# Performance work log

Measured on AMD Instinct MI355X. Metric: run time of the kernel, lower is better.

Reference implementation:

```python
import jax, jax.numpy as jnp
import numpy as np

EPS = 1e-5


def _conv1x1(w, x):
    # w: [O, C, 1, 1], x: [B, C, H, W] -> [B, O, H, W]
    return jnp.einsum('oc,bchw->bohw', w[:, :, 0, 0], x)


def _bn_train(y, g, b):
    # BatchNorm2d in training mode: batch statistics over (B, H, W)
    m = y.mean(axis=(0, 2, 3), keepdims=True)
    v = y.var(axis=(0, 2, 3), keepdims=True)
    return (y - m) * jax.lax.rsqrt(v + EPS) * g[None, :, None, None] + b[None, :, None, None]


def setup_inputs() -> dict:
    key = jax.random.key(0)
    ks = jax.random.split(key, 8)
    B, C, H, W = 16, 512, 32, 32
    width, heads, hd, out_ch = 128, 4, 32, 512  # out_chans*expansion = 512
    return {
        'x': jax.random.normal(ks[0], (B, C, H, W), jnp.float32),
        'conv1_w': jax.random.normal(ks[1], (width, C, 1, 1), jnp.float32) * 0.05,
        'bn1_g': jnp.ones((width,), jnp.float32),
        'bn1_b': jnp.zeros((width,), jnp.float32),
        'qkv_w': jax.random.normal(ks[2], (3 * width, width, 1, 1), jnp.float32) * 0.05,
        'rw': jax.random.normal(ks[3], (1, heads, hd, 1, W), jnp.float32),
        'rh': jax.random.normal(ks[4], (1, heads, hd, H, 1), jnp.float32),
        'conv2_w': jax.random.normal(ks[5], (out_ch, width, 1, 1), jnp.float32) * 0.05,
        'bn2_g': jnp.ones((out_ch,), jnp.float32),
        'bn2_b': jnp.zeros((out_ch,), jnp.float32),
    }


def reference(x, conv1_w, bn1_g, bn1_b, qkv_w, rw, rh, conv2_w, bn2_g, bn2_b):
    B, C, H, W = x.shape
    heads = rw.shape[1]
    width = qkv_w.shape[1]
    hd = width // heads
    scale = hd ** (-0.5)
    N = H * W

    identity = x
    # conv1 = BaseConv: 1x1 conv (no bias) + BN + ReLU
    y = jax.nn.relu(_bn_train(_conv1x1(conv1_w, x), bn1_g, bn1_b))

    # Attention with relative position bias
    qkv = _conv1x1(qkv_w, y)                       # [B, 3*width, H, W]
    qkv = qkv.reshape(B, 3, heads, hd, N)          # split channels as (3, heads, hd)
    q, k, v = qkv[:, 0], qkv[:, 1], qkv[:, 2]      # each [B, heads, hd, N]

    attn_content = jnp.einsum('bhdn,bhdm->bhnm', q, k) * scale  # [B, heads, N, N]
    r = (rw + rh).reshape(heads, hd, N)                          # [heads, hd, N]
    attn_position = jnp.einsum('bhdn,hdm->bhnm', q, r) * scale
    attn = jax.nn.softmax(attn_content + attn_position, axis=-1)
    out = jnp.einsum('bhnm,bhdm->bhdn', attn, v)   # [B, heads, hd, N]
    y = out.reshape(B, width, H, W)

    # conv2 + BN, residual add, ReLU (stride==1: no pooling, no down_sample)
    y = _bn_train(_conv1x1(conv2_w, y), bn2_g, bn2_b)
    y = y + identity
    return jax.nn.relu(y)
```

## Files before the change

### kernel.cpp

```cpp
#include <hip/hip_runtime.h>
#include <cstddef>
#include <cstdint>

constexpr int BATCH = 16;
constexpr int NQ    = 1024;
constexpr float QSCALE = 0.17677669529663687f * 1.4426950408889634f;

typedef __attribute__((ext_vector_type(8))) short bf8;
typedef __attribute__((ext_vector_type(4))) float f32x4;
typedef __attribute__((ext_vector_type(4))) unsigned short us4;
typedef __attribute__((ext_vector_type(8))) unsigned short us8;

__device__ inline unsigned short f2bf(float x) {
  union { float f; uint32_t u; } c{x};
  uint32_t r = c.u + 0x7fffu + ((c.u >> 16) & 1u);
  return (unsigned short)(r >> 16);
}
__device__ inline float b2f(unsigned short v) {
  union { uint32_t u; float f; } c{(uint32_t)v << 16};
  return c.f;
}
__device__ inline float fast_exp2(float x) {
#if __has_builtin(__builtin_amdgcn_exp2f)
  return __builtin_amdgcn_exp2f(x);
#else
  return exp2f(x);
#endif
}

__global__ __launch_bounds__(256) void k_wcvt(const float* __restrict__ w1,
                                              const float* __restrict__ wq,
                                              const float* __restrict__ w2,
                                              unsigned short* __restrict__ o1,
                                              unsigned short* __restrict__ oq,
                                              unsigned short* __restrict__ o2) {
  int idx = (blockIdx.x * 256 + threadIdx.x) * 8;
  const float* s; unsigned short* d; int off;
  if (idx < 65536)        { s = w1; d = o1; off = idx; }
  else if (idx < 114688)  { s = wq; d = oq; off = idx - 65536; }
  else                    { s = w2; d = o2; off = idx - 114688; }
  float4 a = *(const float4*)(s + off);
  float4 b = *(const float4*)(s + off + 4);
  us8 o = {f2bf(a.x), f2bf(a.y), f2bf(a.z), f2bf(a.w),
           f2bf(b.x), f2bf(b.y), f2bf(b.z), f2bf(b.w)};
  *(us8*)(d + off) = o;
}

__global__ __launch_bounds__(256) void k_conv1(const float* __restrict__ x,
                                               const unsigned short* __restrict__ W,
                                               unsigned short* __restrict__ y1T) {
  constexpr int BS = 68;
  __shared__ unsigned short Bl[64 * BS];

  const int bb = blockIdx.z;
  const int n0 = blockIdx.x * 64;
  const int tid = threadIdx.x, lane = tid & 63, wv = tid >> 6;
  const int wn = wv & 1, wm = wv >> 1;
  const int i = lane & 15, g = lane >> 4;

  const int kb = tid >> 4, nb = tid & 15;

  f32x4 acc[2][4];
#pragma unroll
  for (int a = 0; a < 2; ++a)
#pragma unroll
    for (int b = 0; b < 4; ++b) acc[a][b] = {0.f, 0.f, 0.f, 0.f};

  float4 rv[4];
#pragma unroll
  for (int r = 0; r < 4; ++r)
    rv[r] = *(const float4*)(x + (((size_t)(bb * 512 + kb * 4 + r)) << 10) + n0 + nb * 4);

  for (int s = 0; s < 8; ++s) {
    bf8 wf[4][2];
#pragma unroll
    for (int b = 0; b < 4; ++b)
#pragma unroll
      for (int h = 0; h < 2; ++h)
        wf[b][h] = *(const bf8*)(W + (size_t)(wm * 64 + b * 16 + i) * 512 + s * 64 + h * 32 + g * 8);

    __syncthreads();
#pragma unroll
    for (int j = 0; j < 4; ++j) {
      us4 pk = {f2bf((&rv[0].x)[j]), f2bf((&rv[1].x)[j]),
                f2bf((&rv[2].x)[j]), f2bf((&rv[3].x)[j])};
      *(us4*)&Bl[(nb * 4 + j) * BS + kb * 4] = pk;
    }
    __syncthreads();

    if (s < 7) {
#pragma unroll
      for (int r = 0; r < 4; ++r)
        rv[r] = *(const float4*)(x + (((size_t)(bb * 512 + (s + 1) * 64 + kb * 4 + r)) << 10) + n0 + nb * 4);
    }

#pragma unroll
    for (int h = 0; h < 2; ++h) {
      bf8 af[2];
#pragma unroll
      for (int a = 0; a < 2; ++a)
        af[a] = *(const bf8*)&Bl[(wn * 32 + a * 16 + i) * BS + h * 32 + g * 8];
#pragma unroll
      for (int a = 0; a < 2; ++a)
#pragma unroll
        for (int b = 0; b < 4; ++b)
          acc[a][b] = __builtin_amdgcn_mfma_f32_16x16x32_bf16(wf[b][h], af[a], acc[a][b], 0, 0, 0);
    }
  }

#pragma unroll
  for (int a = 0; a < 2; ++a)
#pragma unroll
    for (int b = 0; b < 4; ++b) {
      const int n = n0 + wn * 32 + a * 16 + i;
      const int c = wm * 64 + b * 16 + 4 * g;
      us4 pk = {f2bf(acc[a][b][0]), f2bf(acc[a][b][1]), f2bf(acc[a][b][2]), f2bf(acc[a][b][3])};
      *(us4*)(y1T + ((size_t)(bb << 10) + n) * 128 + c) = pk;
    }
}

template<int KTOT, int MODE>
__global__ __launch_bounds__(256) void k_mm(const unsigned short* __restrict__ W,
                                            const unsigned short* __restrict__ Bact,
                                            const float* __restrict__ scl,
                                            const float* __restrict__ sht,
                                            const float* __restrict__ rw,
                                            const float* __restrict__ rh,
                                            unsigned short* __restrict__ out0,
                                            unsigned short* __restrict__ out1,
                                            unsigned short* __restrict__ out2) {
  constexpr int BS = 136;
  __shared__ unsigned short Blds[128 * BS];
  __shared__ float scl_s[128], sht_s[128];

  const int bb = blockIdx.z, mt = blockIdx.y;
  const int n0 = blockIdx.x * 128, m0 = mt * 64;
  const int tid = threadIdx.x, lane = tid & 63, wv = tid >> 6;
  const int wn = wv & 1, wm = wv >> 1;
  const int i = lane & 15, g = lane >> 4;

  const unsigned short* Bp = Bact + ((size_t)bb * NQ + n0) * KTOT;

  f32x4 acc[4][2];
#pragma unroll
  for (int a = 0; a < 4; ++a)
#pragma unroll
    for (int b = 0; b < 2; ++b) acc[a][b] = {0.f, 0.f, 0.f, 0.f};

  const int sn = tid >> 1;
  const int sk = (tid & 1) * 8;

  if (tid < 128) { scl_s[tid] = scl[tid]; sht_s[tid] = sht[tid]; }
  bf8 wf[2][4];
#pragma unroll
  for (int b = 0; b < 2; ++b)
#pragma unroll
    for (int h = 0; h < 4; ++h)
      wf[b][h] = *(const bf8*)(W + (size_t)(m0 + wm * 32 + b * 16 + i) * 128 + h * 32 + g * 8);
  __syncthreads();
#pragma unroll
  for (int p = 0; p < 8; ++p) {
    us8 v = *(const us8*)(Bp + (size_t)sn * 128 + sk + p * 16);
    const int kb = sk + p * 16;
    float scv[8], shv[8];
    *(float4*)scv = *(const float4*)&scl_s[kb];
    *(float4*)(scv + 4) = *(const float4*)&scl_s[kb + 4];
    *(float4*)shv = *(const float4*)&sht_s[kb];
    *(float4*)(shv + 4) = *(const float4*)&sht_s[kb + 4];
#pragma unroll
    for (int j = 0; j < 8; ++j)
      v[j] = f2bf(fmaxf(fmaf(b2f(v[j]), scv[j], shv[j]), 0.f));
    *(us8*)(&Blds[sn * BS + sk + p * 16]) = v;
  }
  __syncthreads();

  const bool actA = (mt >= 4);
  if (actA) {
#pragma unroll
    for (int h = 0; h < 4; ++h) {
      bf8 af[4];
#pragma unroll
      for (int a = 0; a < 4; ++a)
        af[a] = *(const bf8*)&Blds[(wn * 64 + a * 16 + i) * BS + h * 32 + g * 8];
#pragma unroll
      for (int a = 0; a < 4; ++a)
#pragma unroll
        for (int b = 0; b < 2; ++b)
          acc[a][b] = __builtin_amdgcn_mfma_f32_16x16x32_bf16(af[a], wf[b][h], acc[a][b], 0, 0, 0);
    }
  } else {
#pragma unroll
    for (int h = 0; h < 4; ++h) {
      bf8 af[4];
#pragma unroll
      for (int a = 0; a < 4; ++a)
        af[a] = *(const bf8*)&Blds[(wn * 64 + a * 16 + i) * BS + h * 32 + g * 8];
#pragma unroll
      for (int a = 0; a < 4; ++a)
#pragma unroll
        for (int b = 0; b < 2; ++b)
          acc[a][b] = __builtin_amdgcn_mfma_f32_16x16x32_bf16(wf[b][h], af[a], acc[a][b], 0, 0, 0);
    }
  }

  if (mt < 2) {
#pragma unroll
    for (int a = 0; a < 4; ++a)
#pragma unroll
      for (int b = 0; b < 2; ++b) {
        const int n = n0 + wn * 64 + a * 16 + i;
        const int c = m0 + wm * 32 + b * 16 + 4 * g;
        const int hh = c >> 5, d = c & 31;
        us4 pk = {f2bf(acc[a][b][0] * QSCALE), f2bf(acc[a][b][1] * QSCALE),
                  f2bf(acc[a][b][2] * QSCALE), f2bf(acc[a][b][3] * QSCALE)};
        *(us4*)(out0 + (((size_t)(bb * 4 + hh) << 10) + n) * 32 + d) = pk;
      }
  } else if (mt < 4) {
#pragma unroll
    for (int a = 0; a < 4; ++a)
#pragma unroll
      for (int b = 0; b < 2; ++b) {
        const int n = n0 + wn * 64 + a * 16 + i;
        const int c = (m0 - 128) + wm * 32 + b * 16 + 4 * g;
        const int hh = c >> 5, d = c & 31;
        const int wcol = n & 31, hrow = n >> 5;
        float vv[4];
#pragma unroll
        for (int r = 0; r < 4; ++r)
          vv[r] = acc[a][b][r] + rw[(c + r) * 32 + wcol] + rh[(c + r) * 32 + hrow];
        us4 pk = {f2bf(vv[0]), f2bf(vv[1]), f2bf(vv[2]), f2bf(vv[3])};
        *(us4*)(out1 + (((size_t)(bb * 4 + hh) << 10) + n) * 32 + d) = pk;
      }
  } else {
#pragma unroll
    for (int a = 0; a < 4; ++a)
#pragma unroll
      for (int b = 0; b < 2; ++b) {
        const int c = (m0 - 256) + wm * 32 + b * 16 + i;
        const int nb = n0 + wn * 64 + a * 16 + 4 * g;
        const int hh = c >> 5, dd = c & 31;
        us4 pk = {f2bf(acc[a][b][0]), f2bf(acc[a][b][1]), f2bf(acc[a][b][2]), f2bf(acc[a][b][3])};
        *(us4*)(out2 + (((size_t)(bb * 4 + hh) * 32 + dd) << 10) + nb) = pk;
      }
  }
}

__global__ __launch_bounds__(256) void k_mm2(const unsigned short* __restrict__ W,
                                             const float* __restrict__ Aof,
                                             float* __restrict__ y2,
                                             float* __restrict__ pBS,
                                             float* __restrict__ pBQ) {
  constexpr int BS = 264;
  __shared__ unsigned short Blds[64 * BS];
  __shared__ float Sl[256], Ql[256];
  const int bb = blockIdx.z;
  const int mh = blockIdx.y;
  const int n0 = blockIdx.x * 64;
  const int tid = threadIdx.x, lane = tid & 63, wv = tid >> 6;
  const int wn = wv & 1, wm = wv >> 1;
  const int i = lane & 15, g = lane >> 4;

  Sl[tid] = 0.f; Ql[tid] = 0.f;

  const int sn = tid >> 2, sk = (tid & 3) * 32;
  const float* src = Aof + (((size_t)(bb << 10)) + n0 + sn) * 128 + sk;
#pragma unroll
  for (int p = 0; p < 4; ++p) {
    float4 f0 = *(const float4*)(src + p * 8);
    float4 f1 = *(const float4*)(src + p * 8 + 4);
    float fv[8] = {f0.x, f0.y, f0.z, f0.w, f1.x, f1.y, f1.z, f1.w};
    us8 hi, lo;
#pragma unroll
    for (int j = 0; j < 8; ++j) {
      unsigned short h16 = f2bf(fv[j]);
      hi[j] = h16;
      lo[j] = f2bf(fv[j] - b2f(h16));
    }
    *(us8*)&Blds[sn * BS + sk + p * 8]       = hi;
    *(us8*)&Blds[sn * BS + 128 + sk + p * 8] = lo;
  }
  __syncthreads();

  auto loadw = [&](bf8 (&wf)[2][4], int lp) {
    const int mt = mh * 4 + lp;
#pragma unroll
    for (int b = 0; b < 2; ++b)
#pragma unroll
      for (int h = 0; h < 4; ++h)
        wf[b][h] = *(const bf8*)(W + (size_t)(mt * 64 + wm * 32 + b * 16 + i) * 128 + h * 32 + g * 8);
  };

  auto step = [&](bf8 (&wf)[2][4], int lp) {
    const int mt = mh * 4 + lp;
    f32x4 acc[2][2];
#pragma unroll
    for (int a = 0; a < 2; ++a)
#pragma unroll
      for (int b = 0; b < 2; ++b) acc[a][b] = {0.f, 0.f, 0.f, 0.f};
#pragma unroll
    for (int h = 0; h < 4; ++h) {
      bf8 ah[2], al[2];
#pragma unroll
      for (int a = 0; a < 2; ++a) {
        ah[a] = *(const bf8*)&Blds[(wn * 32 + a * 16 + i) * BS + h * 32 + g * 8];
        al[a] = *(const bf8*)&Blds[(wn * 32 + a * 16 + i) * BS + 128 + h * 32 + g * 8];
      }
#pragma unroll
      for (int a = 0; a < 2; ++a)
#pragma unroll
        for (int b = 0; b < 2; ++b) {
          acc[a][b] = __builtin_amdgcn_mfma_f32_16x16x32_bf16(ah[a], wf[b][h], acc[a][b], 0, 0, 0);
          acc[a][b] = __builtin_amdgcn_mfma_f32_16x16x32_bf16(al[a], wf[b][h], acc[a][b], 0, 0, 0);
        }
    }
#pragma unroll
    for (int a = 0; a < 2; ++a)
#pragma unroll
      for (int b = 0; b < 2; ++b) {
        const int c = mt * 64 + wm * 32 + b * 16 + i;
        const int nb = n0 + wn * 32 + a * 16 + 4 * g;
        *(f32x4*)(y2 + (((size_t)(bb * 512 + c)) << 10) + nb) = acc[a][b];
      }
#pragma unroll
    for (int b = 0; b < 2; ++b) {
      float s = 0.f, q = 0.f;
#pragma unroll
      for (int a = 0; a < 2; ++a)
#pragma unroll
        for (int r = 0; r < 4; ++r) {
          float v = acc[a][b][r];
          s += v; q += v * v;
        }
      s += __shfl_xor(s, 16); s += __shfl_xor(s, 32);
      q += __shfl_xor(q, 16); q += __shfl_xor(q, 32);
      if ((lane & 48) == 0) {
        const int cl = lp * 64 + wm * 32 + b * 16 + i;
        atomicAdd(&Sl[cl], s);
        atomicAdd(&Ql[cl], q);
      }
    }
  };

  bf8 wfA[2][4], wfB[2][4];
  loadw(wfA, 0);
#pragma unroll
  for (int mp = 0; mp < 2; ++mp) {
    loadw(wfB, 2 * mp + 1);
    step(wfA, 2 * mp);
    if (mp < 1) loadw(wfA, 2 * mp + 2);
    step(wfB, 2 * mp + 1);
  }

  __syncthreads();
  const int pidx = bb * 16 + blockIdx.x;
  pBS[(size_t)(mh * 256 + tid) * 256 + pidx] = Sl[tid];
  pBQ[(size_t)(mh * 256 + tid) * 256 + pidx] = Ql[tid];
}

__global__ __launch_bounds__(256) void k_bnstat1a(const unsigned short* __restrict__ y1T,
                                                  float* __restrict__ pS,
                                                  float* __restrict__ pQ) {
  const int blk = blockIdx.x, t = threadIdx.x;
  const int rr = t >> 4, co = t & 15;
  float s[8], q[8];
#pragma unroll
  for (int j = 0; j < 8; ++j) { s[j] = 0.f; q[j] = 0.f; }
  for (int it = 0; it < 16; ++it) {
    const int r = blk * 256 + rr + it * 16;
    us8 v = *(const us8*)(y1T + (size_t)r * 128 + co * 8);
#pragma unroll
    for (int j = 0; j < 8; ++j) { float f = b2f(v[j]); s[j] += f; q[j] += f * f; }
  }
  __shared__ float rs[16][16][8], rq[16][16][8];
#pragma unroll
  for (int j = 0; j < 8; ++j) { rs[rr][co][j] = s[j]; rq[rr][co][j] = q[j]; }
  __syncthreads();
  if (t < 128) {
    const int c = t;
    float S = 0.f, Q = 0.f;
    for (int r2 = 0; r2 < 16; ++r2) { S += rs[r2][c >> 3][c & 7]; Q += rq[r2][c >> 3][c & 7]; }
    pS[c * 64 + blk] = S;
    pQ[c * 64 + blk] = Q;
  }
}

__global__ __launch_bounds__(128) void k_bnfin1(const float* __restrict__ pS,
                                                const float* __restrict__ pQ,
                                                const float* __restrict__ g,
                                                const float* __restrict__ be,
                                                float* __restrict__ scl,
                                                float* __restrict__ sht) {
  const int c = threadIdx.x;
  float S = 0.f, Q = 0.f;
  for (int k = 0; k < 64; ++k) { S += pS[c * 64 + k]; Q += pQ[c * 64 + k]; }
  const float inv_n = 1.f / 16384.f;
  const float mean = S * inv_n, var = Q * inv_n - mean * mean;
  const float sc = rsqrtf(var + 1e-5f) * g[c];
  scl[c] = sc;
  sht[c] = be[c] - mean * sc;
}

__global__ __launch_bounds__(64) void k_bnfin2(const float* __restrict__ pBS,
                                               const float* __restrict__ pBQ,
                                               const float* __restrict__ g,
                                               const float* __restrict__ be,
                                               float* __restrict__ scl,
                                               float* __restrict__ sht) {
  const int c = blockIdx.x, t = threadIdx.x;
  float S = 0.f, Q = 0.f;
#pragma unroll
  for (int k = 0; k < 4; ++k) {
    S += pBS[(size_t)c * 256 + t + k * 64];
    Q += pBQ[(size_t)c * 256 + t + k * 64];
  }
#pragma unroll
  for (int o = 32; o > 0; o >>= 1) {
    S += __shfl_down(S, o);
    Q += __shfl_down(Q, o);
  }
  if (t == 0) {
    const float inv_n = 1.f / 16384.f;
    const float mean = S * inv_n, var = Q * inv_n - mean * mean;
    const float sc = rsqrtf(var + 1e-5f) * g[c];
    scl[c] = sc;
    sht[c] = be[c] - mean * sc;
  }
}

__global__ __launch_bounds__(256) void k_attn_mfma(const unsigned short* __restrict__ qs,
                                                   const unsigned short* __restrict__ kt,
                                                   const unsigned short* __restrict__ vt,
                                                   float* __restrict__ aoT) {
  const int bh   = blockIdx.y;
  const int tid  = threadIdx.x;
  const int lane = tid & 63;
  const int wv   = tid >> 6;
  const int i    = lane & 15;
  const int g    = lane >> 4;
  const int n0w  = blockIdx.x * 64 + wv * 16;

  __shared__ unsigned short Ks[64 * 56];
  __shared__ unsigned short Vt[32 * 72];

  const bf8 qf = *reinterpret_cast<const bf8*>(
      qs + ((size_t)bh * NQ + n0w + i) * 32 + g * 8);

  f32x4 o0 = {0.f, 0.f, 0.f, 0.f}, o1 = {0.f, 0.f, 0.f, 0.f};
  float m = -1e30f, lsum = 0.f;

  const unsigned short* kb = kt + (size_t)bh * NQ * 32;
  const unsigned short* vb = vt + (size_t)bh * 32 * NQ;

  const int skey = tid >> 2, sds = (tid & 3) * 8;
  const int svd  = tid >> 3, svn = (tid & 7) * 8;

  for (int k0 = 0; k0 < NQ; k0 += 64) {
    bf8 kvld = *reinterpret_cast<const bf8*>(kb + (size_t)(k0 + skey) * 32 + sds);
    bf8 vvld = *reinterpret_cast<const bf8*>(vb + (size_t)svd * NQ + k0 + svn);
    __syncthreads();
    *reinterpret_cast<bf8*>(&Ks[skey * 56 + sds]) = kvld;
    *reinterpret_cast<bf8*>(&Vt[svd * 72 + svn])  = vvld;
    __syncthreads();

    f32x4 st[4];
    const f32x4 zero = {0.f, 0.f, 0.f, 0.f};
#pragma unroll
    for (int t = 0; t < 4; ++t) {
      bf8 kf = *reinterpret_cast<const bf8*>(&Ks[(t * 16 + i) * 56 + g * 8]);
      st[t] = __builtin_amdgcn_mfma_f32_16x16x32_bf16(kf, qf, zero, 0, 0, 0);
    }

    float tmax = st[0][0];
#pragma unroll
    for (int t = 0; t < 4; ++t)
#pragma unroll
      for (int r = 0; r < 4; ++r) tmax = fmaxf(tmax, st[t][r]);
    tmax = fmaxf(tmax, __shfl_xor(tmax, 16));
    tmax = fmaxf(tmax, __shfl_xor(tmax, 32));

    const float mn   = fmaxf(m, tmax);
    const float corr = fast_exp2(m - mn);
    m = mn;

    float ps = 0.f;
    unsigned int pk[4][2];
#pragma unroll
    for (int t = 0; t < 4; ++t) {
      float p0 = fast_exp2(st[t][0] - mn);
      float p1 = fast_exp2(st[t][1] - mn);
      float p2 = fast_exp2(st[t][2] - mn);
      float p3 = fast_exp2(st[t][3] - mn);
      ps += (p0 + p1) + (p2 + p3);
      unsigned int pa, pb;
      asm("v_cvt_pk_bf16_f32 %0, %1, %2" : "=v"(pa) : "v"(p0), "v"(p1));
      asm("v_cvt_pk_bf16_f32 %0, %1, %2" : "=v"(pb) : "v"(p2), "v"(p3));
      pk[t][0] = pa; pk[t][1] = pb;
    }
    ps += __shfl_xor(ps, 16);
    ps += __shfl_xor(ps, 32);
    lsum = lsum * corr + ps;
#pragma unroll
    for (int r = 0; r < 4; ++r) { o0[r] *= corr; o1[r] *= corr; }

    const int src0 = ((g & 1) << 5) + i;
    const int src1 = src0 + 16;
    const bool hi = (g >= 2);
#pragma unroll
    for (int s = 0; s < 2; ++s) {
      int a0 = __shfl((int)pk[2 * s][0], src0);
      int a1 = __shfl((int)pk[2 * s][1], src0);
      int a2 = __shfl((int)pk[2 * s][0], src1);
      int a3 = __shfl((int)pk[2 * s][1], src1);
      int b0 = __shfl((int)pk[2 * s + 1][0], src0);
      int b1 = __shfl((int)pk[2 * s + 1][1], src0);
      int b2 = __shfl((int)pk[2 * s + 1][0], src1);
      int b3 = __shfl((int)pk[2 * s + 1][1], src1);
      union { int d[4]; bf8 v; } pf;
      pf.d[0] = hi ? b0 : a0;
      pf.d[1] = hi ? b1 : a1;
      pf.d[2] = hi ? b2 : a2;
      pf.d[3] = hi ? b3 : a3;
      bf8 vf0 = *reinterpret_cast<const bf8*>(&Vt[(i)      * 72 + s * 32 + g * 8]);
      bf8 vf1 = *reinterpret_cast<const bf8*>(&Vt[(16 + i) * 72 + s * 32 + g * 8]);
      o0 = __builtin_amdgcn_mfma_f32_16x16x32_bf16(vf0, pf.v, o0, 0, 0, 0);
      o1 = __builtin_amdgcn_mfma_f32_16x16x32_bf16(vf1, pf.v, o1, 0, 0, 0);
    }
  }

  const float inv = 1.f / lsum;
  float* dst = aoT + (((size_t)(bh >> 2) << 10) + n0w + i) * 128 + (bh & 3) * 32 + 4 * g;
  f32x4 p0 = {o0[0] * inv, o0[1] * inv, o0[2] * inv, o0[3] * inv};
  f32x4 p1 = {o1[0] * inv, o1[1] * inv, o1[2] * inv, o1[3] * inv};
  *(f32x4*)dst        = p0;
  *(f32x4*)(dst + 16) = p1;
}

__global__ __launch_bounds__(256) void k_final(const float* __restrict__ y2,
                                               const float* __restrict__ x,
                                               const float* __restrict__ scl,
                                               const float* __restrict__ sht,
                                               float* __restrict__ out) {
  const size_t idx = ((size_t)blockIdx.x * 256 + threadIdx.x) * 8;
  const int c = (int)((idx >> 10) & 511);
  const float sc = scl[c], sh = sht[c];
  float4 v0 = *(const float4*)(y2 + idx);
  float4 v1 = *(const float4*)(y2 + idx + 4);
  float4 x0 = *(const float4*)(x + idx);
  float4 x1 = *(const float4*)(x + idx + 4);
  float4 o0, o1;
  o0.x = fmaxf(v0.x * sc + sh + x0.x, 0.f);
  o0.y = fmaxf(v0.y * sc + sh + x0.y, 0.f);
  o0.z = fmaxf(v0.z * sc + sh + x0.z, 0.f);
  o0.w = fmaxf(v0.w * sc + sh + x0.w, 0.f);
  o1.x = fmaxf(v1.x * sc + sh + x1.x, 0.f);
  o1.y = fmaxf(v1.y * sc + sh + x1.y, 0.f);
  o1.z = fmaxf(v1.z * sc + sh + x1.z, 0.f);
  o1.w = fmaxf(v1.w * sc + sh + x1.w, 0.f);
  *(float4*)(out + idx)     = o0;
  *(float4*)(out + idx + 4) = o1;
}

extern "C" void kernel_launch(void* const* d_in, const int* in_sizes, int n_in,
                              void* d_out, int out_size, void* d_ws, size_t ws_size,
                              hipStream_t stream) {
  (void)in_sizes; (void)n_in; (void)out_size; (void)ws_size;
  const float* x    = (const float*)d_in[0];
  const float* w1   = (const float*)d_in[1];
  const float* g1   = (const float*)d_in[2];
  const float* b1   = (const float*)d_in[3];
  const float* wqkv = (const float*)d_in[4];
  const float* rw   = (const float*)d_in[5];
  const float* rh   = (const float*)d_in[6];
  const float* w2   = (const float*)d_in[7];
  const float* g2   = (const float*)d_in[8];
  const float* b2   = (const float*)d_in[9];
  float* out = (float*)d_out;
  char* base = (char*)d_ws;

  float*          y2  = (float*)(base);
  unsigned short* y1T = (unsigned short*)(base + (32u << 20));
  unsigned short* qs  = (unsigned short*)(base + (36u << 20));
  unsigned short* kt  = (unsigned short*)(base + (40u << 20));
  unsigned short* vt  = (unsigned short*)(base + (44u << 20));
  float*          aoT = (float*)(base + (48u << 20));
  unsigned short* wb1 = (unsigned short*)(base + (56u << 20));
  unsigned short* wbq = wb1 + 65536;
  unsigned short* wb2 = wbq + 49152;
  float* pS   = (float*)(base + (57u << 20));
  float* pQ   = pS + 8192;
  float* pBS  = pQ + 8192;
  float* pBQ  = pBS + 131072;
  float* scl1 = pBQ + 131072;
  float* sht1 = scl1 + 128;
  float* scl2 = sht1 + 128;
  float* sht2 = scl2 + 512;

  k_wcvt<<<88, 256, 0, stream>>>(w1, wqkv, w2, wb1, wbq, wb2);
  k_conv1<<<dim3(16, 1, BATCH), 256, 0, stream>>>(x, wb1, y1T);
  k_bnstat1a<<<64, 256, 0, stream>>>(y1T, pS, pQ);
  k_bnfin1<<<1, 128, 0, stream>>>(pS, pQ, g1, b1, scl1, sht1);
  k_mm<128, 1><<<dim3(8, 6, BATCH), 256, 0, stream>>>(wbq, y1T, scl1, sht1,
                                                      rw, rh, qs, kt, vt);
  k_attn_mfma<<<dim3(NQ / 64, BATCH * 4), 256, 0, stream>>>(qs, kt, vt, aoT);
  k_mm2<<<dim3(16, 2, BATCH), 256, 0, stream>>>(wb2, aoT, y2, pBS, pBQ);
  k_bnfin2<<<512, 64, 0, stream>>>(pBS, pBQ, g2, b2, scl2, sht2);
  k_final<<<4096, 256, 0, stream>>>(y2, x, scl2, sht2, out);
}
```

Measured before the change: 111.5 us.

## Fuse BN1 stats into conv1 and recompute conv2 to drop y2 buffer

BN1 partial sums are now computed in the conv1 epilogue from the bf16-rounded outputs, which removes the separate k_bnstat1a pass over y1T and parallelises bnfin1 across channels. The conv2 GEMM is run twice: once only for BN2 statistics, and again in a final kernel that applies BN2, the residual and ReLU directly. This avoids writing and re-reading the 32 MB fp32 y2 intermediate. The cost is doubling the conv2 split-bf16 MFMA work and the aoT reads.

```diff
diff --git a/kernel.cpp b/kernel.cpp
--- a/kernel.cpp
+++ b/kernel.cpp
@@ -48,9 +48,12 @@
 
 __global__ __launch_bounds__(256) void k_conv1(const float* __restrict__ x,
                                                const unsigned short* __restrict__ W,
-                                               unsigned short* __restrict__ y1T) {
+                                               unsigned short* __restrict__ y1T,
+                                               float* __restrict__ pS1,
+                                               float* __restrict__ pQ1) {
   constexpr int BS = 68;
   __shared__ unsigned short Bl[64 * BS];
+  __shared__ float Sl[128], Ql[128];
 
   const int bb = blockIdx.z;
   const int n0 = blockIdx.x * 64;
@@ -58,6 +61,8 @@
   const int wn = wv & 1, wm = wv >> 1;
   const int i = lane & 15, g = lane >> 4;
 
+  if (tid < 128) { Sl[tid] = 0.f; Ql[tid] = 0.f; }
+
   const int kb = tid >> 4, nb = tid & 15;
 
   f32x4 acc[2][4];
@@ -117,18 +122,79 @@
       us4 pk = {f2bf(acc[a][b][0]), f2bf(acc[a][b][1]), f2bf(acc[a][b][2]), f2bf(acc[a][b][3])};
       *(us4*)(y1T + ((size_t)(bb << 10) + n) * 128 + c) = pk;
     }
-}
-
-template<int KTOT, int MODE>
-__global__ __launch_bounds__(256) void k_mm(const unsigned short* __restrict__ W,
-                                            const unsigned short* __restrict__ Bact,
-                                            const float* __restrict__ scl,
-                                            const float* __restrict__ sht,
-                                            const float* __restrict__ rw,
-                                            const float* __restrict__ rh,
-                                            unsigned short* __restrict__ out0,
-                                            unsigned short* __restrict__ out1,
-                                            unsigned short* __restrict__ out2) {
+
+#pragma unroll
+  for (int b = 0; b < 4; ++b) {
+    float sb[4], qb[4];
+#pragma unroll
+    for (int r = 0; r < 4; ++r) {
+      float v0 = b2f(f2bf(acc[0][b][r]));
+      float v1 = b2f(f2bf(acc[1][b][r]));
+      sb[r] = v0 + v1;
+      qb[r] = v0 * v0 + v1 * v1;
+    }
+#pragma unroll
+    for (int o = 1; o < 16; o <<= 1) {
+#pragma unroll
+      for (int r = 0; r < 4; ++r) {
+        sb[r] += __shfl_xor(sb[r], o);
+        qb[r] += __shfl_xor(qb[r], o);
+      }
+    }
+    if (i == 0) {
+#pragma unroll
+      for (int r = 0; r < 4; ++r) {
+        const int c = wm * 64 + b * 16 + 4 * g + r;
+        atomicAdd(&Sl[c], sb[r]);
+        atomicAdd(&Ql[c], qb[r]);
+      }
+    }
+  }
+
+  __syncthreads();
+  const int blk = bb * 16 + blockIdx.x;
+  if (tid < 128) {
+    pS1[(size_t)tid * 256 + blk] = Sl[tid];
+    pQ1[(size_t)tid * 256 + blk] = Ql[tid];
+  }
+}
+
+__global__ __launch_bounds__(64) void k_bnfin1(const float* __restrict__ pS1,
+                                               const float* __restrict__ pQ1,
+                                               const float* __restrict__ g,
+                                               const float* __restrict__ be,
+                                               float* __restrict__ scl,
+                                               float* __restrict__ sht) {
+  const int c = blockIdx.x, t = threadIdx.x;
+  float S = 0.f, Q = 0.f;
+#pragma unroll
+  for (int k = 0; k < 4; ++k) {
+    S += pS1[(size_t)c * 256 + t + k * 64];
+    Q += pQ1[(size_t)c * 256 + t + k * 64];
+  }
+#pragma unroll
+  for (int o = 32; o > 0; o >>= 1) {
+    S += __shfl_down(S, o);
+    Q += __shfl_down(Q, o);
+  }
+  if (t == 0) {
+    const float inv_n = 1.f / 16384.f;
+    const float mean = S * inv_n, var = Q * inv_n - mean * mean;
+    const float sc = rsqrtf(var + 1e-5f) * g[c];
+    scl[c] = sc;
+    sht[c] = be[c] - mean * sc;
+  }
+}
+
+__global__ __launch_bounds__(256) void k_qkv(const unsigned short* __restrict__ W,
+                                             const unsigned short* __restrict__ Bact,
+                                             const float* __restrict__ scl,
+                                             const float* __restrict__ sht,
+                                             const float* __restrict__ rw,
+                                             const float* __restrict__ rh,
+                                             unsigned short* __restrict__ out0,
+                                             unsigned short* __restrict__ out1,
+                                             unsigned short* __restrict__ out2) {
   constexpr int BS = 136;
   __shared__ unsigned short Blds[128 * BS];
   __shared__ float scl_s[128], sht_s[128];
@@ -139,7 +205,7 @@
   const int wn = wv & 1, wm = wv >> 1;
   const int i = lane & 15, g = lane >> 4;
 
-  const unsigned short* Bp = Bact + ((size_t)bb * NQ + n0) * KTOT;
+  const unsigned short* Bp = Bact + ((size_t)bb * NQ + n0) * 128;
 
   f32x4 acc[4][2];
 #pragma unroll
@@ -242,188 +308,6 @@
         us4 pk = {f2bf(acc[a][b][0]), f2bf(acc[a][b][1]), f2bf(acc[a][b][2]), f2bf(acc[a][b][3])};
         *(us4*)(out2 + (((size_t)(bb * 4 + hh) * 32 + dd) << 10) + nb) = pk;
       }
-  }
-}
-
-__global__ __launch_bounds__(256) void k_mm2(const unsigned short* __restrict__ W,
-                                             const float* __restrict__ Aof,
-                                             float* __restrict__ y2,
-                                             float* __restrict__ pBS,
-                                             float* __restrict__ pBQ) {
-  constexpr int BS = 264;
-  __shared__ unsigned short Blds[64 * BS];
-  __shared__ float Sl[256], Ql[256];
-  const int bb = blockIdx.z;
-  const int mh = blockIdx.y;
-  const int n0 = blockIdx.x * 64;
-  const int tid = threadIdx.x, lane = tid & 63, wv = tid >> 6;
-  const int wn = wv & 1, wm = wv >> 1;
-  const int i = lane & 15, g = lane >> 4;
-
-  Sl[tid] = 0.f; Ql[tid] = 0.f;
-
-  const int sn = tid >> 2, sk = (tid & 3) * 32;
-  const float* src = Aof + (((size_t)(bb << 10)) + n0 + sn) * 128 + sk;
-#pragma unroll
-  for (int p = 0; p < 4; ++p) {
-    float4 f0 = *(const float4*)(src + p * 8);
-    float4 f1 = *(const float4*)(src + p * 8 + 4);
-    float fv[8] = {f0.x, f0.y, f0.z, f0.w, f1.x, f1.y, f1.z, f1.w};
-    us8 hi, lo;
-#pragma unroll
-    for (int j = 0; j < 8; ++j) {
-      unsigned short h16 = f2bf(fv[j]);
-      hi[j] = h16;
-      lo[j] = f2bf(fv[j] - b2f(h16));
-    }
-    *(us8*)&Blds[sn * BS + sk + p * 8]       = hi;
-    *(us8*)&Blds[sn * BS + 128 + sk + p * 8] = lo;
-  }
-  __syncthreads();
-
-  auto loadw = [&](bf8 (&wf)[2][4], int lp) {
-    const int mt = mh * 4 + lp;
-#pragma unroll
-    for (int b = 0; b < 2; ++b)
-#pragma unroll
-      for (int h = 0; h < 4; ++h)
-        wf[b][h] = *(const bf8*)(W + (size_t)(mt * 64 + wm * 32 + b * 16 + i) * 128 + h * 32 + g * 8);
-  };
-
-  auto step = [&](bf8 (&wf)[2][4], int lp) {
-    const int mt = mh * 4 + lp;
-    f32x4 acc[2][2];
-#pragma unroll
-    for (int a = 0; a < 2; ++a)
-#pragma unroll
-      for (int b = 0; b < 2; ++b) acc[a][b] = {0.f, 0.f, 0.f, 0.f};
-#pragma unroll
-    for (int h = 0; h < 4; ++h) {
-      bf8 ah[2], al[2];
-#pragma unroll
-      for (int a = 0; a < 2; ++a) {
-        ah[a] = *(const bf8*)&Blds[(wn * 32 + a * 16 + i) * BS + h * 32 + g * 8];
-        al[a] = *(const bf8*)&Blds[(wn * 32 + a * 16 + i) * BS + 128 + h * 32 + g * 8];
-      }
-#pragma unroll
-      for (int a = 0; a < 2; ++a)
-#pragma unroll
-        for (int b = 0; b < 2; ++b) {
-          acc[a][b] = __builtin_amdgcn_mfma_f32_16x16x32_bf16(ah[a], wf[b][h], acc[a][b], 0, 0, 0);
-          acc[a][b] = __builtin_amdgcn_mfma_f32_16x16x32_bf16(al[a], wf[b][h], acc[a][b], 0, 0, 0);
-        }
-    }
-#pragma unroll
-    for (int a = 0; a < 2; ++a)
-#pragma unroll
-      for (int b = 0; b < 2; ++b) {
-        const int c = mt * 64 + wm * 32 + b * 16 + i;
-        const int nb = n0 + wn * 32 + a * 16 + 4 * g;
-        *(f32x4*)(y2 + (((size_t)(bb * 512 + c)) << 10) + nb) = acc[a][b];
-      }
-#pragma unroll
-    for (int b = 0; b < 2; ++b) {
-      float s = 0.f, q = 0.f;
-#pragma unroll
-      for (int a = 0; a < 2; ++a)
-#pragma unroll
-        for (int r = 0; r < 4; ++r) {
-          float v = acc[a][b][r];
-          s += v; q += v * v;
-        }
-      s += __shfl_xor(s, 16); s += __shfl_xor(s, 32);
-      q += __shfl_xor(q, 16); q += __shfl_xor(q, 32);
-      if ((lane & 48) == 0) {
-        const int cl = lp * 64 + wm * 32 + b * 16 + i;
-        atomicAdd(&Sl[cl], s);
-        atomicAdd(&Ql[cl], q);
-      }
-    }
-  };
-
-  bf8 wfA[2][4], wfB[2][4];
-  loadw(wfA, 0);
-#pragma unroll
-  for (int mp = 0; mp < 2; ++mp) {
-    loadw(wfB, 2 * mp + 1);
-    step(wfA, 2 * mp);
-    if (mp < 1) loadw(wfA, 2 * mp + 2);
-    step(wfB, 2 * mp + 1);
-  }
-
-  __syncthreads();
-  const int pidx = bb * 16 + blockIdx.x;
-  pBS[(size_t)(mh * 256 + tid) * 256 + pidx] = Sl[tid];
-  pBQ[(size_t)(mh * 256 + tid) * 256 + pidx] = Ql[tid];
-}
-
-__global__ __launch_bounds__(256) void k_bnstat1a(const unsigned short* __restrict__ y1T,
-                                                  float* __restrict__ pS,
-                                                  float* __restrict__ pQ) {
-  const int blk = blockIdx.x, t = threadIdx.x;
-  const int rr = t >> 4, co = t & 15;
-  float s[8], q[8];
-#pragma unroll
-  for (int j = 0; j < 8; ++j) { s[j] = 0.f; q[j] = 0.f; }
-  for (int it = 0; it < 16; ++it) {
-    const int r = blk * 256 + rr + it * 16;
-    us8 v = *(const us8*)(y1T + (size_t)r * 128 + co * 8);
-#pragma unroll
-    for (int j = 0; j < 8; ++j) { float f = b2f(v[j]); s[j] += f; q[j] += f * f; }
-  }
-  __shared__ float rs[16][16][8], rq[16][16][8];
-#pragma unroll
-  for (int j = 0; j < 8; ++j) { rs[rr][co][j] = s[j]; rq[rr][co][j] = q[j]; }
-  __syncthreads();
-  if (t < 128) {
-    const int c = t;
-    float S = 0.f, Q = 0.f;
-    for (int r2 = 0; r2 < 16; ++r2) { S += rs[r2][c >> 3][c & 7]; Q += rq[r2][c >> 3][c & 7]; }
-    pS[c * 64 + blk] = S;
-    pQ[c * 64 + blk] = Q;
-  }
-}
-
-__global__ __launch_bounds__(128) void k_bnfin1(const float* __restrict__ pS,
-                                                const float* __restrict__ pQ,
-                                                const float* __restrict__ g,
-                                                const float* __restrict__ be,
-                                                float* __restrict__ scl,
-                                                float* __restrict__ sht) {
-  const int c = threadIdx.x;
-  float S = 0.f, Q = 0.f;
-  for (int k = 0; k < 64; ++k) { S += pS[c * 64 + k]; Q += pQ[c * 64 + k]; }
-  const float inv_n = 1.f / 16384.f;
-  const float mean = S * inv_n, var = Q * inv_n - mean * mean;
-  const float sc = rsqrtf(var + 1e-5f) * g[c];
-  scl[c] = sc;
-  sht[c] = be[c] - mean * sc;
-}
-
-__global__ __launch_bounds__(64) void k_bnfin2(const float* __restrict__ pBS,
-                                               const float* __restrict__ pBQ,
-                                               const float* __restrict__ g,
-                                               const float* __restrict__ be,
-                                               float* __restrict__ scl,
-                                               float* __restrict__ sht) {
-  const int c = blockIdx.x, t = threadIdx.x;
-  float S = 0.f, Q = 0.f;
-#pragma unroll
-  for (int k = 0; k < 4; ++k) {
-    S += pBS[(size_t)c * 256 + t + k * 64];
-    Q += pBQ[(size_t)c * 256 + t + k * 64];
-  }
-#pragma unroll
-  for (int o = 32; o > 0; o >>= 1) {
-    S += __shfl_down(S, o);
-    Q += __shfl_down(Q, o);
-  }
-  if (t == 0) {
-    const float inv_n = 1.f / 16384.f;
-    const float mean = S * inv_n, var = Q * inv_n - mean * mean;
-    const float sc = rsqrtf(var + 1e-5f) * g[c];
-    scl[c] = sc;
-    sht[c] = be[c] - mean * sc;
   }
 }
 
@@ -535,29 +419,233 @@
   *(f32x4*)(dst + 16) = p1;
 }
 
-__global__ __launch_bounds__(256) void k_final(const float* __restrict__ y2,
-                                               const float* __restrict__ x,
-                                               const float* __restrict__ scl,
-                                               const float* __restrict__ sht,
-                                               float* __restrict__ out) {
-  const size_t idx = ((size_t)blockIdx.x * 256 + threadIdx.x) * 8;
-  const int c = (int)((idx >> 10) & 511);
-  const float sc = scl[c], sh = sht[c];
-  float4 v0 = *(const float4*)(y2 + idx);
-  float4 v1 = *(const float4*)(y2 + idx + 4);
-  float4 x0 = *(const float4*)(x + idx);
-  float4 x1 = *(const float4*)(x + idx + 4);
-  float4 o0, o1;
-  o0.x = fmaxf(v0.x * sc + sh + x0.x, 0.f);
-  o0.y = fmaxf(v0.y * sc + sh + x0.y, 0.f);
-  o0.z = fmaxf(v0.z * sc + sh + x0.z, 0.f);
-  o0.w = fmaxf(v0.w * sc + sh + x0.w, 0.f);
-  o1.x = fmaxf(v1.x * sc + sh + x1.x, 0.f);
-  o1.y = fmaxf(v1.y * sc + sh + x1.y, 0.f);
-  o1.z = fmaxf(v1.z * sc + sh + x1.z, 0.f);
-  o1.w = fmaxf(v1.w * sc + sh + x1.w, 0.f);
-  *(float4*)(out + idx)     = o0;
-  *(float4*)(out + idx + 4) = o1;
+__global__ __launch_bounds__(256) void k_stat2(const unsigned short* __restrict__ W,
+                                               const float* __restrict__ Aof,
+                                               float* __restrict__ pBS,
+                                               float* __restrict__ pBQ) {
+  constexpr int BS = 264;
+  __shared__ unsigned short Blds[64 * BS];
+  __shared__ float Sl[256], Ql[256];
+  const int bb = blockIdx.z;
+  const int mh = blockIdx.y;
+  const int n0 = blockIdx.x * 64;
+  const int tid = threadIdx.x, lane = tid & 63, wv = tid >> 6;
+  const int wn = wv & 1, wm = wv >> 1;
+  const int i = lane & 15, g = lane >> 4;
+
+  Sl[tid] = 0.f; Ql[tid] = 0.f;
+
+  const int sn = tid >> 2, sk = (tid & 3) * 32;
+  const float* src = Aof + (((size_t)(bb << 10)) + n0 + sn) * 128 + sk;
+#pragma unroll
+  for (int p = 0; p < 4; ++p) {
+    float4 f0 = *(const float4*)(src + p * 8);
+    float4 f1 = *(const float4*)(src + p * 8 + 4);
+    float fv[8] = {f0.x, f0.y, f0.z, f0.w, f1.x, f1.y, f1.z, f1.w};
+    us8 hi, lo;
+#pragma unroll
+    for (int j = 0; j < 8; ++j) {
+      unsigned short h16 = f2bf(fv[j]);
+      hi[j] = h16;
+      lo[j] = f2bf(fv[j] - b2f(h16));
+    }
+    *(us8*)&Blds[sn * BS + sk + p * 8]       = hi;
+    *(us8*)&Blds[sn * BS + 128 + sk + p * 8] = lo;
+  }
+  __syncthreads();
+
+  auto loadw = [&](bf8 (&wf)[2][4], int lp) {
+    const int mt = mh * 4 + lp;
+#pragma unroll
+    for (int b = 0; b < 2; ++b)
+#pragma unroll
+      for (int h = 0; h < 4; ++h)
+        wf[b][h] = *(const bf8*)(W + (size_t)(mt * 64 + wm * 32 + b * 16 + i) * 128 + h * 32 + g * 8);
+  };
+
+  auto step = [&](bf8 (&wf)[2][4], int lp) {
+    f32x4 acc[2][2];
+#pragma unroll
+    for (int a = 0; a < 2; ++a)
+#pragma unroll
+      for (int b = 0; b < 2; ++b) acc[a][b] = {0.f, 0.f, 0.f, 0.f};
+#pragma unroll
+    for (int h = 0; h < 4; ++h) {
+      bf8 ah[2], al[2];
+#pragma unroll
+      for (int a = 0; a < 2; ++a) {
+        ah[a] = *(const bf8*)&Blds[(wn * 32 + a * 16 + i) * BS + h * 32 + g * 8];
+        al[a] = *(const bf8*)&Blds[(wn * 32 + a * 16 + i) * BS + 128 + h * 32 + g * 8];
+      }
+#pragma unroll
+      for (int a = 0; a < 2; ++a)
+#pragma unroll
+        for (int b = 0; b < 2; ++b) {
+          acc[a][b] = __builtin_amdgcn_mfma_f32_16x16x32_bf16(ah[a], wf[b][h], acc[a][b], 0, 0, 0);
+          acc[a][b] = __builtin_amdgcn_mfma_f32_16x16x32_bf16(al[a], wf[b][h], acc[a][b], 0, 0, 0);
+        }
+    }
+#pragma unroll
+    for (int b = 0; b < 2; ++b) {
+      float s = 0.f, q = 0.f;
+#pragma unroll
+      for (int a = 0; a < 2; ++a)
+#pragma unroll
+        for (int r = 0; r < 4; ++r) {
+          float v = acc[a][b][r];
+          s += v; q += v * v;
+        }
+      s += __shfl_xor(s, 16); s += __shfl_xor(s, 32);
+      q += __shfl_xor(q, 16); q += __shfl_xor(q, 32);
+      if ((lane & 48) == 0) {
+        const int cl = lp * 64 + wm * 32 + b * 16 + i;
+        atomicAdd(&Sl[cl], s);
+        atomicAdd(&Ql[cl], q);
+      }
+    }
+  };
+
+  bf8 wfA[2][4], wfB[2][4];
+  loadw(wfA, 0);
+  loadw(wfB, 1);
+  step(wfA, 0);
+  loadw(wfA, 2);
+  step(wfB, 1);
+  loadw(wfB, 3);
+  step(wfA, 2);
+  step(wfB, 3);
+
+  __syncthreads();
+  const int pidx = bb * 16 + blockIdx.x;
+  pBS[(size_t)(mh * 256 + tid) * 256 + pidx] = Sl[tid];
+  pBQ[(size_t)(mh * 256 + tid) * 256 + pidx] = Ql[tid];
+}
+
+__global__ __launch_bounds__(64) void k_bnfin2(const float* __restrict__ pBS,
+                                               const float* __restrict__ pBQ,
+                                               const float* __restrict__ g,
+                                               const float* __restrict__ be,
+                                               float* __restrict__ scl,
+                                               float* __restrict__ sht) {
+  const int c = blockIdx.x, t = threadIdx.x;
+  float S = 0.f, Q = 0.f;
+#pragma unroll
+  for (int k = 0; k < 4; ++k) {
+    S += pBS[(size_t)c * 256 + t + k * 64];
+    Q += pBQ[(size_t)c * 256 + t + k * 64];
+  }
+#pragma unroll
+  for (int o = 32; o > 0; o >>= 1) {
+    S += __shfl_down(S, o);
+    Q += __shfl_down(Q, o);
+  }
+  if (t == 0) {
+    const float inv_n = 1.f / 16384.f;
+    const float mean = S * inv_n, var = Q * inv_n - mean * mean;
+    const float sc = rsqrtf(var + 1e-5f) * g[c];
+    scl[c] = sc;
+    sht[c] = be[c] - mean * sc;
+  }
+}
+
+__global__ __launch_bounds__(256) void k_final2(const unsigned short* __restrict__ W,
+                                                const float* __restrict__ Aof,
+                                                const float* __restrict__ x,
+                                                const float* __restrict__ scl2,
+                                                const float* __restrict__ sht2,
+                                                float* __restrict__ out) {
+  constexpr int BS = 264;
+  __shared__ unsigned short Blds[64 * BS];
+  __shared__ float scl_s[256], sht_s[256];
+  const int bb = blockIdx.z;
+  const int mh = blockIdx.y;
+  const int n0 = blockIdx.x * 64;
+  const int tid = threadIdx.x, lane = tid & 63, wv = tid >> 6;
+  const int wn = wv & 1, wm = wv >> 1;
+  const int i = lane & 15, g = lane >> 4;
+
+  scl_s[tid] = scl2[mh * 256 + tid];
+  sht_s[tid] = sht2[mh * 256 + tid];
+
+  const int sn = tid >> 2, sk = (tid & 3) * 32;
+  const float* src = Aof + (((size_t)(bb << 10)) + n0 + sn) * 128 + sk;
+#pragma unroll
+  for (int p = 0; p < 4; ++p) {
+    float4 f0 = *(const float4*)(src + p * 8);
+    float4 f1 = *(const float4*)(src + p * 8 + 4);
+    float fv[8] = {f0.x, f0.y, f0.z, f0.w, f1.x, f1.y, f1.z, f1.w};
+    us8 hi, lo;
+#pragma unroll
+    for (int j = 0; j < 8; ++j) {
+      unsigned short h16 = f2bf(fv[j]);
+      hi[j] = h16;
+      lo[j] = f2bf(fv[j] - b2f(h16));
+    }
+    *(us8*)&Blds[sn * BS + sk + p * 8]       = hi;
+    *(us8*)&Blds[sn * BS + 128 + sk + p * 8] = lo;
+  }
+  __syncthreads();
+
+  auto loadw = [&](bf8 (&wf)[2][4], int lp) {
+    const int mt = mh * 4 + lp;
+#pragma unroll
+    for (int b = 0; b < 2; ++b)
+#pragma unroll
+      for (int h = 0; h < 4; ++h)
+        wf[b][h] = *(const bf8*)(W + (size_t)(mt * 64 + wm * 32 + b * 16 + i) * 128 + h * 32 + g * 8);
+  };
+
+  auto step = [&](bf8 (&wf)[2][4], int lp) {
+    const int mt = mh * 4 + lp;
+    f32x4 acc[2][2];
+#pragma unroll
+    for (int a = 0; a < 2; ++a)
+#pragma unroll
+      for (int b = 0; b < 2; ++b) acc[a][b] = {0.f, 0.f, 0.f, 0.f};
+#pragma unroll
+    for (int h = 0; h < 4; ++h) {
+      bf8 ah[2], al[2];
+#pragma unroll
+      for (int a = 0; a < 2; ++a) {
+        ah[a] = *(const bf8*)&Blds[(wn * 32 + a * 16 + i) * BS + h * 32 + g * 8];
+        al[a] = *(const bf8*)&Blds[(wn * 32 + a * 16 + i) * BS + 128 + h * 32 + g * 8];
+      }
+#pragma unroll
+      for (int a = 0; a < 2; ++a)
+#pragma unroll
+        for (int b = 0; b < 2; ++b) {
+          acc[a][b] = __builtin_amdgcn_mfma_f32_16x16x32_bf16(ah[a], wf[b][h], acc[a][b], 0, 0, 0);
+          acc[a][b] = __builtin_amdgcn_mfma_f32_16x16x32_bf16(al[a], wf[b][h], acc[a][b], 0, 0, 0);
+        }
+    }
+#pragma unroll
+    for (int a = 0; a < 2; ++a)
+#pragma unroll
+      for (int b = 0; b < 2; ++b) {
+        const int c = mt * 64 + wm * 32 + b * 16 + i;
+        const int cl = lp * 64 + wm * 32 + b * 16 + i;
+        const int nb = n0 + wn * 32 + a * 16 + 4 * g;
+        const float sc = scl_s[cl], sh = sht_s[cl];
+        const size_t off = (((size_t)(bb * 512 + c)) << 10) + nb;
+        float4 xv = *(const float4*)(x + off);
+        f32x4 o;
+        o[0] = fmaxf(acc[a][b][0] * sc + sh + xv.x, 0.f);
+        o[1] = fmaxf(acc[a][b][1] * sc + sh + xv.y, 0.f);
+        o[2] = fmaxf(acc[a][b][2] * sc + sh + xv.z, 0.f);
+        o[3] = fmaxf(acc[a][b][3] * sc + sh + xv.w, 0.f);
+        *(f32x4*)(out + off) = o;
+      }
+  };
+
+  bf8 wfA[2][4], wfB[2][4];
+  loadw(wfA, 0);
+  loadw(wfB, 1);
+  step(wfA, 0);
+  loadw(wfA, 2);
+  step(wfB, 1);
+  loadw(wfB, 3);
+  step(wfA, 2);
+  step(wfB, 3);
 }
 
 extern "C" void kernel_launch(void* const* d_in, const int* in_sizes, int n_in,
@@ -577,18 +665,17 @@
   float* out = (float*)d_out;
   char* base = (char*)d_ws;
 
-  float*          y2  = (float*)(base);
-  unsigned short* y1T = (unsigned short*)(base + (32u << 20));
-  unsigned short* qs  = (unsigned short*)(base + (36u << 20));
-  unsigned short* kt  = (unsigned short*)(base + (40u << 20));
-  unsigned short* vt  = (unsigned short*)(base + (44u << 20));
-  float*          aoT = (float*)(base + (48u << 20));
-  unsigned short* wb1 = (unsigned short*)(base + (56u << 20));
+  float*          aoT = (float*)(base);
+  unsigned short* y1T = (unsigned short*)(base + (8u  << 20));
+  unsigned short* qs  = (unsigned short*)(base + (12u << 20));
+  unsigned short* kt  = (unsigned short*)(base + (16u << 20));
+  unsigned short* vt  = (unsigned short*)(base + (20u << 20));
+  unsigned short* wb1 = (unsigned short*)(base + (24u << 20));
   unsigned short* wbq = wb1 + 65536;
   unsigned short* wb2 = wbq + 49152;
-  float* pS   = (float*)(base + (57u << 20));
-  float* pQ   = pS + 8192;
-  float* pBS  = pQ + 8192;
+  float* pS1  = (float*)(base + (25u << 20));
+  float* pQ1  = pS1 + 32768;
+  float* pBS  = pQ1 + 32768;
   float* pBQ  = pBS + 131072;
   float* scl1 = pBQ + 131072;
   float* sht1 = scl1 + 128;
@@ -596,13 +683,12 @@
   float* sht2 = scl2 + 512;
 
   k_wcvt<<<88, 256, 0, stream>>>(w1, wqkv, w2, wb1, wbq, wb2);
-  k_conv1<<<dim3(16, 1, BATCH), 256, 0, stream>>>(x, wb1, y1T);
-  k_bnstat1a<<<64, 256, 0, stream>>>(y1T, pS, pQ);
-  k_bnfin1<<<1, 128, 0, stream>>>(pS, pQ, g1, b1, scl1, sht1);
-  k_mm<128, 1><<<dim3(8, 6, BATCH), 256, 0, stream>>>(wbq, y1T, scl1, sht1,
-                                                      rw, rh, qs, kt, vt);
+  k_conv1<<<dim3(16, 1, BATCH), 256, 0, stream>>>(x, wb1, y1T, pS1, pQ1);
+  k_bnfin1<<<128, 64, 0, stream>>>(pS1, pQ1, g1, b1, scl1, sht1);
+  k_qkv<<<dim3(8, 6, BATCH), 256, 0, stream>>>(wbq, y1T, scl1, sht1,
+                                               rw, rh, qs, kt, vt);
   k_attn_mfma<<<dim3(NQ / 64, BATCH * 4), 256, 0, stream>>>(qs, kt, vt, aoT);
-  k_mm2<<<dim3(16, 2, BATCH), 256, 0, stream>>>(wb2, aoT, y2, pBS, pBQ);
+  k_stat2<<<dim3(16, 2, BATCH), 256, 0, stream>>>(wb2, aoT, pBS, pBQ);
   k_bnfin2<<<512, 64, 0, stream>>>(pBS, pBQ, g2, b2, scl2, sht2);
-  k_final<<<4096, 256, 0, stream>>>(y2, x, scl2, sht2, out);
-}
+  k_final2<<<dim3(16, 2, BATCH), 256, 0, stream>>>(wb2, aoT, x, scl2, sht2, out);
+}
```

Result: faster. 107.7 us (-3.4%).
